# Optimization experiments

Hardware: AMD Instinct MI355X
Metric: run time of the kernel (lower is better)

## Reference

```python
import jax, jax.numpy as jnp
import numpy as np

ROUTINGS = 3
EPS = 1e-7  # tf.keras.backend.epsilon()


def _squash(s):
    # s: (B, num_caps, cap_dim)
    n = jnp.linalg.norm(s, axis=-1, keepdims=True)
    return (n ** 2 / (1.0 + n ** 2)) * s / (n + EPS)


def setup_inputs() -> dict:
    key = jax.random.key(0)
    k1, k2 = jax.random.split(key)
    B, N, D_IN, M, C = 64, 2048, 16, 32, 16
    inputs = jax.random.normal(k1, (B, N, D_IN), dtype=jnp.float32)
    # he_normal: std = sqrt(2 / fan_in), fan_in = D_IN for the (1, D_IN, M*C) kernel
    W = jax.random.normal(k2, (D_IN, M, C), dtype=jnp.float32) * np.float32(np.sqrt(2.0 / D_IN))
    return {"inputs": inputs, "W": W}


def reference(inputs, W):
    # prediction vectors u_hat: (B, N, num_caps, cap_dim)
    u_hat = jnp.einsum('bnd,dmc->bnmc', inputs, W)
    b = jnp.zeros(u_hat.shape[:3], dtype=u_hat.dtype)  # (B, N, num_caps)
    v = None
    for _ in range(ROUTINGS):  # fixed small routing count
        c = jax.nn.softmax(b, axis=1)                      # over input capsules
        s = jnp.einsum('bnm,bnmc->bmc', c, u_hat)          # weighted sum
        v = _squash(s)                                     # (B, num_caps, cap_dim)
        b = b + jnp.einsum('bmc,bnmc->bnm', v, u_hat)      # agreement update
    return v
```

## Files before the change

kernel.cpp:

```cpp
#include <hip/hip_runtime.h>
#include <math.h>


#define TPB 1024
#define LOG2E 1.44269504088896f

typedef __attribute__((ext_vector_type(8))) short short8;
typedef __attribute__((ext_vector_type(4))) float float4v;
typedef __attribute__((ext_vector_type(4))) unsigned uint4v;

#define DPP_ADDF(x, ctrl) \
    ((x) + __int_as_float(__builtin_amdgcn_update_dpp( \
        0, __float_as_int(x), (ctrl), 0xF, 0xF, true)))

static __device__ inline unsigned short f2bf(float x) {
    unsigned u = __float_as_uint(x);
    return (unsigned short)((u + 0x7FFFu + ((u >> 16) & 1u)) >> 16);
}
static __device__ inline unsigned pk2(float a, float b) {
    return (unsigned)f2bf(a) | ((unsigned)f2bf(b) << 16);
}

__global__ __launch_bounds__(TPB, 2)
void capsule_routing_kernel(const float* __restrict__ in,
                            const float* __restrict__ W,
                            float* __restrict__ out)
{
    __shared__ unsigned short innorm[2048 * 16];
    __shared__ unsigned short inT[16 * 2056];
    __shared__ float scratch[16][320];
    __shared__ unsigned short cumT[16 * 24];

    const int tid  = threadIdx.x;
    const int w    = tid >> 6;
    const int l    = tid & 63;
    const int ml   = l & 15;
    const int quad = l >> 4;
    const int b    = blockIdx.x & 63;
    const int m0g  = (blockIdx.x >> 6) << 4;

    {
        const float4* gin = (const float4*)(in + ((size_t)b << 15));
        const int d0   = (tid & 3) * 4;
        const int g    = tid >> 2;
        const int n0   = g << 3;
        const int rot2 = (g & 3) << 1;
        float c0 = 0.f, c1 = 0.f, c2 = 0.f, c3 = 0.f;
        unsigned pk32[4][4];
        #pragma unroll
        for (int k = 0; k < 8; ++k) {
            const int n = n0 + ((k + rot2) & 7);
            const float4 gv = gin[n * 4 + (tid & 3)];
            c0 += gv.x; c1 += gv.y; c2 += gv.z; c3 += gv.w;
            const unsigned short u0 = f2bf(gv.x), u1 = f2bf(gv.y),
                                 u2 = f2bf(gv.z), u3 = f2bf(gv.w);
            uint2 pkr; pkr.x = (unsigned)u0 | ((unsigned)u1 << 16);
                       pkr.y = (unsigned)u2 | ((unsigned)u3 << 16);
            *(uint2*)&innorm[n * 16 + d0] = pkr;
            const int j = k >> 1;
            if ((k & 1) == 0) {
                pk32[0][j] = u0; pk32[1][j] = u1;
                pk32[2][j] = u2; pk32[3][j] = u3;
            } else {
                pk32[0][j] |= (unsigned)u0 << 16; pk32[1][j] |= (unsigned)u1 << 16;
                pk32[2][j] |= (unsigned)u2 << 16; pk32[3][j] |= (unsigned)u3 << 16;
            }
        }
        #pragma unroll
        for (int j = 0; j < 4; ++j) {
            const int nn = n0 + ((2 * j + rot2) & 7);
            *(unsigned*)&inT[(d0 + 0) * 2056 + nn] = pk32[0][j];
            *(unsigned*)&inT[(d0 + 1) * 2056 + nn] = pk32[1][j];
            *(unsigned*)&inT[(d0 + 2) * 2056 + nn] = pk32[2][j];
            *(unsigned*)&inT[(d0 + 3) * 2056 + nn] = pk32[3][j];
        }
        c0 = DPP_ADDF(c0, 0x104); c0 = DPP_ADDF(c0, 0x108);
        c1 = DPP_ADDF(c1, 0x104); c1 = DPP_ADDF(c1, 0x108);
        c2 = DPP_ADDF(c2, 0x104); c2 = DPP_ADDF(c2, 0x108);
        c3 = DPP_ADDF(c3, 0x104); c3 = DPP_ADDF(c3, 0x108);
        if ((l & 15) < 4) {
            float4 v4; v4.x = c0; v4.y = c1; v4.z = c2; v4.w = c3;
            *(float4*)&scratch[w][quad * 20 + (l & 3) * 4] = v4;
        }
    }

    float cwv = 0.f;

    for (int pass = 0; pass < 3; ++pass) {
        if (pass) {
            short8 bc = {0,0,0,0,0,0,0,0};
            if (quad < 2)
                bc = *(const short8*)&cumT[ml * 24 + quad * 8];
            float4v xc = {0.f, 0.f, 0.f, 0.f};
            float Sp = 0.f;
            unsigned short* ew = (unsigned short*)&scratch[w][0];

            #pragma unroll 2
            for (int t = 0; t < 4; ++t) {
                const int nb = (w << 7) + (t << 5);
                short8 a0 = {0,0,0,0,0,0,0,0};
                short8 a1 = {0,0,0,0,0,0,0,0};
                if (quad < 2) {
                    a0 = *(const short8*)&innorm[(nb + ml) * 16 + quad * 8];
                    a1 = *(const short8*)&innorm[(nb + 16 + ml) * 16 + quad * 8];
                }
                const float4v z = {0.f, 0.f, 0.f, 0.f};
                float4v c0 = __builtin_amdgcn_mfma_f32_16x16x32_bf16(a0, bc, z, 0, 0, 0);
                float4v c1 = __builtin_amdgcn_mfma_f32_16x16x32_bf16(a1, bc, z, 0, 0, 0);
                float e00 = exp2f(c0[0]), e01 = exp2f(c0[1]),
                      e02 = exp2f(c0[2]), e03 = exp2f(c0[3]);
                float e10 = exp2f(c1[0]), e11 = exp2f(c1[1]),
                      e12 = exp2f(c1[2]), e13 = exp2f(c1[3]);
                Sp += (e00 + e01) + (e02 + e03) + (e10 + e11) + (e12 + e13);
                uint4v ewv;
                ewv[0] = pk2(e00, e01); ewv[1] = pk2(e02, e03);
                ewv[2] = pk2(e10, e11); ewv[3] = pk2(e12, e13);
                *(uint4v*)&ew[ml * 40 + quad * 8] = ewv;
                union { uint2 u2v[2]; short8 s; } ua;
                const int ub = ml * 40 + (quad & 1) * 16 + ((quad >> 1) << 2);
                ua.u2v[0] = *(const uint2*)&ew[ub];
                ua.u2v[1] = *(const uint2*)&ew[ub + 8];
                const short8 bi = *(const short8*)&inT[ml * 2056 + nb + quad * 8];
                xc = __builtin_amdgcn_mfma_f32_16x16x32_bf16(ua.s, bi, xc, 0, 0, 0);
            }
            Sp += __shfl_xor(Sp, 16);
            Sp += __shfl_xor(Sp, 32);
            #pragma unroll
            for (int r = 0; r < 4; ++r)
                scratch[w][(quad * 4 + r) * 17 + ml] = xc[r];
            if (l < 16) scratch[w][272 + l] = Sp;
        }
        __syncthreads();

        if (tid < 256) {
            const int m  = tid >> 4;
            const int tc = tid & 15;
            const int lbase = tid & 48;
            float Stot, xtot = 0.f;
            if (pass == 0) {
                Stot = 2048.f;
                #pragma unroll 4
                for (int w2 = 0; w2 < 16; ++w2)
                    #pragma unroll
                    for (int q = 0; q < 4; ++q)
                        xtot += scratch[w2][q * 20 + tc];
            } else {
                Stot = 0.f;
                #pragma unroll 4
                for (int w2 = 0; w2 < 16; ++w2) {
                    Stot += scratch[w2][272 + m];
                    xtot += scratch[w2][m * 17 + tc];
                }
            }
            float s = 0.f;
            #pragma unroll
            for (int d = 0; d < 16; ++d)
                s += __shfl(xtot, lbase + d) * W[(d << 9) + ((m0g + m) << 4) + tc];
            s /= Stot;
            float n2 = s * s;
            n2 += __shfl_xor(n2, 1);
            n2 += __shfl_xor(n2, 2);
            n2 += __shfl_xor(n2, 4);
            n2 += __shfl_xor(n2, 8);
            const float nr = sqrtf(n2);
            const float v  = s * (n2 / (1.f + n2)) / (nr + 1e-7f);
            if (pass < 2) {
                const float4* Wrow = (const float4*)&W[(tc << 9) + ((m0g + m) << 4)];
                float wvv = 0.f;
                #pragma unroll
                for (int c4 = 0; c4 < 4; ++c4) {
                    const float4 wf = Wrow[c4];
                    wvv += wf.x * __shfl(v, lbase + c4 * 4 + 0)
                         + wf.y * __shfl(v, lbase + c4 * 4 + 1)
                         + wf.z * __shfl(v, lbase + c4 * 4 + 2)
                         + wf.w * __shfl(v, lbase + c4 * 4 + 3);
                }
                cwv += wvv;
                cumT[m * 24 + tc] = f2bf(cwv * LOG2E);
            } else {
                out[((size_t)b << 9) + ((m0g + m) << 4) + tc] = v;
            }
        }
        if (pass < 2) __syncthreads();
    }
}

extern "C" void kernel_launch(void* const* d_in, const int* in_sizes, int n_in,
                              void* d_out, int out_size, void* d_ws, size_t ws_size,
                              hipStream_t stream) {
    (void)in_sizes; (void)n_in; (void)d_ws; (void)ws_size; (void)out_size;
    const float* in = (const float*)d_in[0];
    const float* W  = (const float*)d_in[1];
    float* out = (float*)d_out;
    hipLaunchKernelGGL(capsule_routing_kernel, dim3(128), dim3(TPB), 0, stream,
                       in, W, out);
}
```

Measured before the change: 70.33 us.

## Hoist MFMA operands into registers, shuffle exp weights, drop innorm LDS

```diff
diff --git a/kernel.cpp b/kernel.cpp
--- a/kernel.cpp
+++ b/kernel.cpp
@@ -6,8 +6,14 @@
 #define LOG2E 1.44269504088896f
 
 typedef __attribute__((ext_vector_type(8))) short short8;
+typedef __attribute__((ext_vector_type(4))) short short4v;
 typedef __attribute__((ext_vector_type(4))) float float4v;
-typedef __attribute__((ext_vector_type(4))) unsigned uint4v;
+
+#if defined(__has_builtin)
+#if __has_builtin(__builtin_amdgcn_mfma_f32_16x16x16bf16_1k)
+#define HAVE_MFMA16 1
+#endif
+#endif
 
 #define DPP_ADDF(x, ctrl) \
     ((x) + __int_as_float(__builtin_amdgcn_update_dpp( \
@@ -26,10 +32,10 @@
                             const float* __restrict__ W,
                             float* __restrict__ out)
 {
-    __shared__ unsigned short innorm[2048 * 16];
     __shared__ unsigned short inT[16 * 2056];
     __shared__ float scratch[16][320];
     __shared__ unsigned short cumT[16 * 24];
+    __shared__ float tbx[4][64];
 
     const int tid  = threadIdx.x;
     const int w    = tid >> 6;
@@ -39,8 +45,9 @@
     const int b    = blockIdx.x & 63;
     const int m0g  = (blockIdx.x >> 6) << 4;
 
+    const float4* gin4 = (const float4*)(in + ((size_t)b << 15));
+
     {
-        const float4* gin = (const float4*)(in + ((size_t)b << 15));
         const int d0   = (tid & 3) * 4;
         const int g    = tid >> 2;
         const int n0   = g << 3;
@@ -50,13 +57,10 @@
         #pragma unroll
         for (int k = 0; k < 8; ++k) {
             const int n = n0 + ((k + rot2) & 7);
-            const float4 gv = gin[n * 4 + (tid & 3)];
+            const float4 gv = gin4[n * 4 + (tid & 3)];
             c0 += gv.x; c1 += gv.y; c2 += gv.z; c3 += gv.w;
             const unsigned short u0 = f2bf(gv.x), u1 = f2bf(gv.y),
                                  u2 = f2bf(gv.z), u3 = f2bf(gv.w);
-            uint2 pkr; pkr.x = (unsigned)u0 | ((unsigned)u1 << 16);
-                       pkr.y = (unsigned)u2 | ((unsigned)u3 << 16);
-            *(uint2*)&innorm[n * 16 + d0] = pkr;
             const int j = k >> 1;
             if ((k & 1) == 0) {
                 pk32[0][j] = u0; pk32[1][j] = u1;
@@ -78,50 +82,104 @@
         c1 = DPP_ADDF(c1, 0x104); c1 = DPP_ADDF(c1, 0x108);
         c2 = DPP_ADDF(c2, 0x104); c2 = DPP_ADDF(c2, 0x108);
         c3 = DPP_ADDF(c3, 0x104); c3 = DPP_ADDF(c3, 0x108);
-        if ((l & 15) < 4) {
+        c0 += __shfl_xor(c0, 16); c0 += __shfl_xor(c0, 32);
+        c1 += __shfl_xor(c1, 16); c1 += __shfl_xor(c1, 32);
+        c2 += __shfl_xor(c2, 16); c2 += __shfl_xor(c2, 32);
+        c3 += __shfl_xor(c3, 16); c3 += __shfl_xor(c3, 32);
+        if (l < 4) {
             float4 v4; v4.x = c0; v4.y = c1; v4.z = c2; v4.w = c3;
-            *(float4*)&scratch[w][quad * 20 + (l & 3) * 4] = v4;
+            *(float4*)&scratch[w][l * 4] = v4;
         }
     }
+
+#ifdef HAVE_MFMA16
+    short4v a0h[4], a1h[4];
+#else
+    short8 a0h[4], a1h[4];
+#endif
+    short8 bih[4];
+    #pragma unroll
+    for (int t = 0; t < 4; ++t) {
+        const int nb = (w << 7) + (t << 5);
+#ifdef HAVE_MFMA16
+        {
+            const float4 ga = gin4[(nb + ml) * 4 + quad];
+            const float4 gb = gin4[(nb + 16 + ml) * 4 + quad];
+            short4v a; a[0] = (short)f2bf(ga.x); a[1] = (short)f2bf(ga.y);
+                       a[2] = (short)f2bf(ga.z); a[3] = (short)f2bf(ga.w);
+            short4v c; c[0] = (short)f2bf(gb.x); c[1] = (short)f2bf(gb.y);
+                       c[2] = (short)f2bf(gb.z); c[3] = (short)f2bf(gb.w);
+            a0h[t] = a; a1h[t] = c;
+        }
+#else
+        {
+            short8 a = {0,0,0,0,0,0,0,0}, c = {0,0,0,0,0,0,0,0};
+            if (quad < 2) {
+                const float4 g0 = gin4[(nb + ml) * 4 + quad * 2];
+                const float4 g1 = gin4[(nb + ml) * 4 + quad * 2 + 1];
+                const float4 h0 = gin4[(nb + 16 + ml) * 4 + quad * 2];
+                const float4 h1 = gin4[(nb + 16 + ml) * 4 + quad * 2 + 1];
+                a[0]=(short)f2bf(g0.x); a[1]=(short)f2bf(g0.y);
+                a[2]=(short)f2bf(g0.z); a[3]=(short)f2bf(g0.w);
+                a[4]=(short)f2bf(g1.x); a[5]=(short)f2bf(g1.y);
+                a[6]=(short)f2bf(g1.z); a[7]=(short)f2bf(g1.w);
+                c[0]=(short)f2bf(h0.x); c[1]=(short)f2bf(h0.y);
+                c[2]=(short)f2bf(h0.z); c[3]=(short)f2bf(h0.w);
+                c[4]=(short)f2bf(h1.x); c[5]=(short)f2bf(h1.y);
+                c[6]=(short)f2bf(h1.z); c[7]=(short)f2bf(h1.w);
+            }
+            a0h[t] = a; a1h[t] = c;
+        }
+#endif
+        bih[t] = *(const short8*)&inT[ml * 2056 + nb + quad * 8];
+    }
+
+    const int srcAB = ml + ((quad == 0) ? 16 : (quad == 1) ? 32 : 0);
+    const int srcCD = ml + ((quad == 1) ? 48 : (quad == 3) ? 32 : 16);
+    const bool selAB = (quad == 1) || (quad == 2);
+    const bool selC  = (quad == 3);
 
     float cwv = 0.f;
 
     for (int pass = 0; pass < 3; ++pass) {
         if (pass) {
+#ifdef HAVE_MFMA16
+            const short4v bc = *(const short4v*)&cumT[ml * 24 + quad * 4];
+#else
             short8 bc = {0,0,0,0,0,0,0,0};
             if (quad < 2)
                 bc = *(const short8*)&cumT[ml * 24 + quad * 8];
+#endif
             float4v xc = {0.f, 0.f, 0.f, 0.f};
             float Sp = 0.f;
-            unsigned short* ew = (unsigned short*)&scratch[w][0];
-
-            #pragma unroll 2
+
+            #pragma unroll
             for (int t = 0; t < 4; ++t) {
-                const int nb = (w << 7) + (t << 5);
-                short8 a0 = {0,0,0,0,0,0,0,0};
-                short8 a1 = {0,0,0,0,0,0,0,0};
-                if (quad < 2) {
-                    a0 = *(const short8*)&innorm[(nb + ml) * 16 + quad * 8];
-                    a1 = *(const short8*)&innorm[(nb + 16 + ml) * 16 + quad * 8];
-                }
                 const float4v z = {0.f, 0.f, 0.f, 0.f};
-                float4v c0 = __builtin_amdgcn_mfma_f32_16x16x32_bf16(a0, bc, z, 0, 0, 0);
-                float4v c1 = __builtin_amdgcn_mfma_f32_16x16x32_bf16(a1, bc, z, 0, 0, 0);
+#ifdef HAVE_MFMA16
+                float4v c0 = __builtin_amdgcn_mfma_f32_16x16x16bf16_1k(a0h[t], bc, z, 0, 0, 0);
+                float4v c1 = __builtin_amdgcn_mfma_f32_16x16x16bf16_1k(a1h[t], bc, z, 0, 0, 0);
+#else
+                float4v c0 = __builtin_amdgcn_mfma_f32_16x16x32_bf16(a0h[t], bc, z, 0, 0, 0);
+                float4v c1 = __builtin_amdgcn_mfma_f32_16x16x32_bf16(a1h[t], bc, z, 0, 0, 0);
+#endif
                 float e00 = exp2f(c0[0]), e01 = exp2f(c0[1]),
                       e02 = exp2f(c0[2]), e03 = exp2f(c0[3]);
                 float e10 = exp2f(c1[0]), e11 = exp2f(c1[1]),
                       e12 = exp2f(c1[2]), e13 = exp2f(c1[3]);
                 Sp += (e00 + e01) + (e02 + e03) + (e10 + e11) + (e12 + e13);
-                uint4v ewv;
-                ewv[0] = pk2(e00, e01); ewv[1] = pk2(e02, e03);
-                ewv[2] = pk2(e10, e11); ewv[3] = pk2(e12, e13);
-                *(uint4v*)&ew[ml * 40 + quad * 8] = ewv;
-                union { uint2 u2v[2]; short8 s; } ua;
-                const int ub = ml * 40 + (quad & 1) * 16 + ((quad >> 1) << 2);
-                ua.u2v[0] = *(const uint2*)&ew[ub];
-                ua.u2v[1] = *(const uint2*)&ew[ub + 8];
-                const short8 bi = *(const short8*)&inT[ml * 2056 + nb + quad * 8];
-                xc = __builtin_amdgcn_mfma_f32_16x16x32_bf16(ua.s, bi, xc, 0, 0, 0);
+                const unsigned d00 = pk2(e00, e01), d01 = pk2(e02, e03);
+                const unsigned d10 = pk2(e10, e11), d11 = pk2(e12, e13);
+                const unsigned RA = (unsigned)__shfl((int)(selAB ? d00 : d10), srcAB);
+                const unsigned RB = (unsigned)__shfl((int)(selAB ? d01 : d11), srcAB);
+                const unsigned RC = (unsigned)__shfl((int)(selC  ? d00 : d10), srcCD);
+                const unsigned RD = (unsigned)__shfl((int)(selC  ? d01 : d11), srcCD);
+                union { unsigned u[4]; short8 s; } ua;
+                ua.u[0] = (quad == 0) ? d00 : (selC ? RC : RA);
+                ua.u[1] = (quad == 0) ? d01 : (selC ? RD : RB);
+                ua.u[2] = (quad == 0) ? RA  : (selC ? d10 : RC);
+                ua.u[3] = (quad == 0) ? RB  : (selC ? d11 : RD);
+                xc = __builtin_amdgcn_mfma_f32_16x16x32_bf16(ua.s, bih[t], xc, 0, 0, 0);
             }
             Sp += __shfl_xor(Sp, 16);
             Sp += __shfl_xor(Sp, 32);
@@ -135,27 +193,36 @@
         if (tid < 256) {
             const int m  = tid >> 4;
             const int tc = tid & 15;
-            const int lbase = tid & 48;
+            const int wt = tid >> 6;
+            const int mr = m & 3;
             float Stot, xtot = 0.f;
             if (pass == 0) {
                 Stot = 2048.f;
-                #pragma unroll 4
+                #pragma unroll
                 for (int w2 = 0; w2 < 16; ++w2)
-                    #pragma unroll
-                    for (int q = 0; q < 4; ++q)
-                        xtot += scratch[w2][q * 20 + tc];
+                    xtot += scratch[w2][tc];
             } else {
                 Stot = 0.f;
-                #pragma unroll 4
+                #pragma unroll
                 for (int w2 = 0; w2 < 16; ++w2) {
                     Stot += scratch[w2][272 + m];
                     xtot += scratch[w2][m * 17 + tc];
                 }
             }
-            float s = 0.f;
-            #pragma unroll
-            for (int d = 0; d < 16; ++d)
-                s += __shfl(xtot, lbase + d) * W[(d << 9) + ((m0g + m) << 4) + tc];
+            tbx[wt][mr * 16 + tc] = xtot;
+            const float4 x0 = *(const float4*)&tbx[wt][mr * 16 + 0];
+            const float4 x1 = *(const float4*)&tbx[wt][mr * 16 + 4];
+            const float4 x2 = *(const float4*)&tbx[wt][mr * 16 + 8];
+            const float4 x3 = *(const float4*)&tbx[wt][mr * 16 + 12];
+            const float* Wb = &W[((m0g + m) << 4) + tc];
+            float s = x0.x * Wb[0 << 9]  + x0.y * Wb[1 << 9]
+                    + x0.z * Wb[2 << 9]  + x0.w * Wb[3 << 9]
+                    + x1.x * Wb[4 << 9]  + x1.y * Wb[5 << 9]
+                    + x1.z * Wb[6 << 9]  + x1.w * Wb[7 << 9]
+                    + x2.x * Wb[8 << 9]  + x2.y * Wb[9 << 9]
+                    + x2.z * Wb[10 << 9] + x2.w * Wb[11 << 9]
+                    + x3.x * Wb[12 << 9] + x3.y * Wb[13 << 9]
+                    + x3.z * Wb[14 << 9] + x3.w * Wb[15 << 9];
             s /= Stot;
             float n2 = s * s;
             n2 += __shfl_xor(n2, 1);
@@ -165,16 +232,17 @@
             const float nr = sqrtf(n2);
             const float v  = s * (n2 / (1.f + n2)) / (nr + 1e-7f);
             if (pass < 2) {
+                tbx[wt][mr * 16 + tc] = v;
+                const float4 v0 = *(const float4*)&tbx[wt][mr * 16 + 0];
+                const float4 v1 = *(const float4*)&tbx[wt][mr * 16 + 4];
+                const float4 v2 = *(const float4*)&tbx[wt][mr * 16 + 8];
+                const float4 v3 = *(const float4*)&tbx[wt][mr * 16 + 12];
                 const float4* Wrow = (const float4*)&W[(tc << 9) + ((m0g + m) << 4)];
-                float wvv = 0.f;
-                #pragma unroll
-                for (int c4 = 0; c4 < 4; ++c4) {
-                    const float4 wf = Wrow[c4];
-                    wvv += wf.x * __shfl(v, lbase + c4 * 4 + 0)
-                         + wf.y * __shfl(v, lbase + c4 * 4 + 1)
-                         + wf.z * __shfl(v, lbase + c4 * 4 + 2)
-                         + wf.w * __shfl(v, lbase + c4 * 4 + 3);
-                }
+                const float4 w0 = Wrow[0], w1 = Wrow[1], w2 = Wrow[2], w3 = Wrow[3];
+                float wvv = w0.x * v0.x + w0.y * v0.y + w0.z * v0.z + w0.w * v0.w
+                          + w1.x * v1.x + w1.y * v1.y + w1.z * v1.z + w1.w * v1.w
+                          + w2.x * v2.x + w2.y * v2.y + w2.z * v2.z + w2.w * v2.w
+                          + w3.x * v3.x + w3.y * v3.y + w3.z * v3.z + w3.w * v3.w;
                 cwv += wvv;
                 cumT[m * 24 + tc] = f2bf(cwv * LOG2E);
             } else {
```

After: 70.81 us. No clear change (+0.7%).
